# Kernel optimization log

Hardware: AMD Instinct MI355X
Metric: run time of the kernel (lower is better)

Reference implementation:

```python
import jax, jax.numpy as jnp
import numpy as np

CLAMP_MIN = -1.0
CLAMP_MAX = 1.0
EPS = 1e-5


def setup_inputs() -> dict:
    key = jax.random.key(0)
    k1, k2, k3, k4 = jax.random.split(key, 4)
    x = jax.random.normal(k1, (16, 3, 64, 64, 64), dtype=jnp.float32)
    w = jax.random.normal(k2, (16, 3, 3, 3, 3), dtype=jnp.float32) * 0.11  # ~kaiming scale for fan_in=81
    b = jax.random.normal(k3, (16,), dtype=jnp.float32) * 0.1
    m = jax.random.normal(k4, (16, 1, 1, 1), dtype=jnp.float32)
    return {"x": x, "w": w, "b": b, "m": m}


def reference(x, w, b, m):
    # Valid 3D conv: [N,3,D,H,W] x [16,3,3,3,3] -> [N,16,D-2,H-2,W-2]
    y = jax.lax.conv_general_dilated(
        x, w, window_strides=(1, 1, 1), padding='VALID',
        dimension_numbers=('NCDHW', 'OIDHW', 'NCDHW'))
    y = y + b[None, :, None, None, None]
    y = y * m[None]  # per-channel multiply before instance norm
    # InstanceNorm3d (affine=False, biased variance) over spatial dims per (n, c)
    mu = jnp.mean(y, axis=(2, 3, 4), keepdims=True)
    var = jnp.var(y, axis=(2, 3, 4), keepdims=True)
    y = (y - mu) * jax.lax.rsqrt(var + EPS)
    # clamp, second per-channel multiply, then max over channel dim
    y = jnp.clip(y, CLAMP_MIN, CLAMP_MAX) * m[None]
    return jnp.max(y, axis=1)  # [N, D-2, H-2, W-2]
```

## Files before the change

kernel.cpp:

```cpp
#include <hip/hip_runtime.h>
#include <hip/hip_bf16.h>
#include <float.h>

#define DI   64
#define DOUT 62
#define CI   3
#define CO   16
#define NB   16
constexpr int SP    = DOUT * DOUT * DOUT;
constexpr int SP64  = DOUT * DOUT * 64;
constexpr int HT    = 31;
constexpr int DT    = 16;
constexpr int NPART = HT * DT;
constexpr int XDW   = NB * CI * DI * DI * DI / 2;
constexpr int RSTR  = 34;
constexpr int PHD   = 72 * RSTR;

typedef __attribute__((ext_vector_type(8))) short bf16x8;
typedef __attribute__((ext_vector_type(4))) float f32x4;

__device__ float g_psum[NB * CO * NPART];
__device__ float g_psq [NB * CO * NPART];
__device__ float g_stats[NB * CO * 2];
__device__ uint4 g_wb4[4 * 64];
__device__ uint2 g_rt [4 * 64];
__device__ unsigned int g_xbf[XDW];

__device__ __forceinline__ unsigned short f2bf(float v) {
    __hip_bfloat16 h = __float2bfloat16(v);
    return __builtin_bit_cast(unsigned short, h);
}
__device__ __forceinline__ unsigned int pk2(float lo, float hi) {
    return (unsigned int)f2bf(lo) | ((unsigned int)f2bf(hi) << 16);
}

__global__ __launch_bounds__(256) void x2bf_kernel(const float* __restrict__ x,
                                                   const float* __restrict__ w)
{
    if (blockIdx.x == 0) {
        unsigned int* dst = (unsigned int*)g_wb4;
        for (int dwi = threadIdx.x; dwi < 4 * 64 * 4; dwi += 256) {
            const int t    = dwi >> 8;
            const int lane = (dwi >> 2) & 63;
            const int dw   = dwi & 3;
            const int o    = lane & 15, q = lane >> 4;
            const int P    = t * 4 + q;
            unsigned int u = 0;
            for (int half = 0; half < 2; ++half) {
                const int j = dw * 2 + half;
                const int g = (j < 4) ? (2 * P) : (2 * P + 1);
                const int r = j & 3;
                float val = 0.f;
                if (g <= 26 && r < 3) {
                    const int i = g / 9, kd = (g % 9) / 3, kh = g % 3;
                    val = w[o * 81 + i * 27 + kd * 9 + kh * 3 + r];
                }
                u |= ((unsigned int)f2bf(val)) << (16 * half);
            }
            dst[dwi] = u;
        }
        if (threadIdx.x < 256) {
            const int t = threadIdx.x >> 6, lane = threadIdx.x & 63;
            const int q = lane >> 4, P = t * 4 + q;
            uint2 rt;
            const int gA = 2 * P, gB = 2 * P + 1;
            rt.x = (gA <= 26) ? ((gA / 9) * 24 + ((gA % 9) / 3) * 4 + gA % 3) * RSTR : 0;
            rt.y = (gB <= 26) ? ((gB / 9) * 24 + ((gB % 9) / 3) * 4 + gB % 3) * RSTR : 0;
            g_rt[t * 64 + lane] = rt;
        }
    }
    int i = blockIdx.x * 256 + threadIdx.x;
    const int stride = gridDim.x * 256;
    for (; i < XDW / 2; i += stride) {
        const float4 v = ((const float4*)x)[i];
        uint2 u;
        u.x = pk2(v.x, v.y);
        u.y = pk2(v.z, v.w);
        ((uint2*)g_xbf)[i] = u;
    }
}

template <int MODE>
__global__ __launch_bounds__(512) void conv_mfma_kernel(
    const float* __restrict__ m,
    unsigned int* __restrict__ y32, float* __restrict__ out)
{
    __shared__ unsigned int xs[4 * PHD];
    __shared__ float redS[8][CO], redQ[8][CO];

    const int lane = threadIdx.x, ty = threadIdx.y;
    const int h0 = blockIdx.x * 2, d0 = blockIdx.y * 4, n = blockIdx.z;
    const int tid = ty * 64 + lane;

    for (int idx = tid; idx < 72 * 16; idx += 512) {
        const int row = idx >> 4, t = (idx & 15) * 2;
        const int i = row / 24, rm = row % 24, p = rm >> 2, hr = rm & 3;
        const int dg = min(d0 + p, DI - 1);
        const uint2 u = *(const uint2*)(g_xbf +
                          (((n * CI + i) * DI + dg) * DI + (h0 + hr)) * 32 + t);
        const unsigned D2 = __shfl_down(u.x, 1);
        const unsigned D3 = __shfl_down(u.y, 1);
        const unsigned a10 = __builtin_amdgcn_alignbit(u.y, u.x, 16);
        const unsigned a21 = __builtin_amdgcn_alignbit(D2, u.y, 16);
        const unsigned a32 = __builtin_amdgcn_alignbit(D3, D2, 16);
        unsigned int* dp = xs + row * RSTR + t;
        *(uint2*)(dp + 0 * PHD) = u;
        *(uint2*)(dp + 1 * PHD) = make_uint2(a10, a21);
        *(uint2*)(dp + 2 * PHD) = make_uint2(u.y, D2);
        *(uint2*)(dp + 3 * PHD) = make_uint2(a21, a32);
    }
    __syncthreads();

    const int c = lane & 15, q = lane >> 4;
    const int dl = ty >> 1, hl = ty & 1;
    const int offr = ((dl << 2) + hl) * RSTR;

    bf16x8 wf[4];
    int aA[4], aB[4];
#pragma unroll
    for (int t = 0; t < 4; ++t) {
        wf[t] = __builtin_bit_cast(bf16x8, g_wb4[t * 64 + lane]);
        const uint2 rt = g_rt[t * 64 + lane];
        aA[t] = (int)rt.x + offr + 2 * c;
        aB[t] = (int)rt.y + offr + 2 * c;
    }

    const float mc = m[c];
    float A = 0.f, Bp = 0.f;
    if (MODE == 2) {
        A  = g_stats[(n * CO + c) * 2 + 0];
        Bp = g_stats[(n * CO + c) * 2 + 1];
    }

    const int d = d0 + dl, h = h0 + hl;
    const bool dvalid = d < DOUT;
    float sS = 0.f, qS = 0.f;

    if (dvalid) {
        f32x4 acc[4];
#pragma unroll
        for (int wt = 0; wt < 4; ++wt) {
            f32x4 a = {0.f, 0.f, 0.f, 0.f};
#pragma unroll
            for (int t = 0; t < 4; ++t) {
                const uint2 lo = *(const uint2*)(xs + wt * PHD + aA[t]);
                const uint2 hi = *(const uint2*)(xs + wt * PHD + aB[t]);
                uint4 av;
                av.x = lo.x; av.y = lo.y; av.z = hi.x; av.w = hi.y;
                a = __builtin_amdgcn_mfma_f32_16x16x32_bf16(
                        __builtin_bit_cast(bf16x8, av), wf[t], a, 0, 0, 0);
            }
            acc[wt] = a;
        }

        if (MODE == 2) {
            const size_t spb = (size_t)(d * DOUT + h) * DOUT + 16 * q;
#pragma unroll
            for (int reg = 0; reg < 4; ++reg)
#pragma unroll
                for (int wt = 0; wt < 4; ++wt) {
                    const int p = reg * 4 + wt;
                    float z = fminf(fmaxf(fmaf(acc[wt][reg], A, Bp), -1.f), 1.f) * mc;
                    z = fmaxf(z, __shfl_xor(z, 1));
                    z = fmaxf(z, __shfl_xor(z, 2));
                    z = fmaxf(z, __shfl_xor(z, 4));
                    z = fmaxf(z, __shfl_xor(z, 8));
                    if (c == p && (p < 14 || q < 3))
                        out[(size_t)n * SP + spb + p] = z;
                }
        } else {
#pragma unroll
            for (int wt = 0; wt < 4; ++wt)
#pragma unroll
                for (int reg = 0; reg < 4; ++reg) {
                    const float a = acc[wt][reg];
                    sS += a; qS = fmaf(a, a, qS);
                }
            if (q == 3) {
                const float e2 = acc[2][3], e3 = acc[3][3];
                sS -= e2 + e3;
                qS -= fmaf(e2, e2, e3 * e3);
            }
            if (MODE == 1) {
                const size_t ypd = (size_t)(n * CO + c) * (SP64 / 2)
                                 + (size_t)(d * DOUT + h) * 32 + 8 * q;
                uint4 s0, s1;
                s0.x = pk2(acc[0][0], acc[1][0]); s0.y = pk2(acc[2][0], acc[3][0]);
                s0.z = pk2(acc[0][1], acc[1][1]); s0.w = pk2(acc[2][1], acc[3][1]);
                s1.x = pk2(acc[0][2], acc[1][2]); s1.y = pk2(acc[2][2], acc[3][2]);
                s1.z = pk2(acc[0][3], acc[1][3]); s1.w = pk2(acc[2][3], acc[3][3]);
                *(uint4*)(y32 + ypd)     = s0;
                *(uint4*)(y32 + ypd + 4) = s1;
            }
        }
    }

    if (MODE != 2) {
        sS += __shfl_xor(sS, 16); qS += __shfl_xor(qS, 16);
        sS += __shfl_xor(sS, 32); qS += __shfl_xor(qS, 32);
        if (lane < 16) { redS[ty][c] = sS; redQ[ty][c] = qS; }
        __syncthreads();
        if (ty == 0 && lane < 16) {
            float s = 0.f, qq = 0.f;
#pragma unroll
            for (int wv = 0; wv < 8; ++wv) { s += redS[wv][lane]; qq += redQ[wv][lane]; }
            const int blk = blockIdx.y * HT + blockIdx.x;
            g_psum[(n * CO + lane) * NPART + blk] = s;
            g_psq [(n * CO + lane) * NPART + blk] = qq;
        }
    }
}

__global__ __launch_bounds__(256) void finalize_stats_kernel(const float* __restrict__ m)
{
    const int idx = blockIdx.x;
    const int tid = threadIdx.x;
    __shared__ float ls[256], lq[256];
    float s = g_psum[idx * NPART + tid];
    float q = g_psq [idx * NPART + tid];
    if (tid + 256 < NPART) {
        s += g_psum[idx * NPART + tid + 256];
        q += g_psq [idx * NPART + tid + 256];
    }
    ls[tid] = s; lq[tid] = q;
    __syncthreads();
    for (int off = 128; off > 0; off >>= 1) {
        if (tid < off) { ls[tid] += ls[tid + off]; lq[tid] += lq[tid + off]; }
        __syncthreads();
    }
    if (tid == 0) {
        const float inv_n = 1.0f / (float)SP;
        const float muA = ls[0] * inv_n;
        const float varA = fmaxf(lq[0] * inv_n - muA * muA, 0.f);
        const float mo = m[idx & 15];
        const float isv = rsqrtf(fmaf(mo * mo, varA, 1e-5f));
        const float A = mo * isv;
        g_stats[idx * 2 + 0] = A;
        g_stats[idx * 2 + 1] = -muA * A;
    }
}

__global__ __launch_bounds__(256) void pass2_kernel(
    const unsigned int* __restrict__ y32, const float* __restrict__ m,
    float* __restrict__ out)
{
    const int n = blockIdx.y;
    const int t2 = blockIdx.x * 256 + threadIdx.x;
    if (t2 >= DOUT * DOUT * 16) return;
    const int wp2 = t2 & 15;
    const int row = t2 >> 4;
    const float* st = g_stats + n * CO * 2;
    const uint2* yn = (const uint2*)(y32 + (size_t)n * CO * (SP64 / 2)) + t2;
    float mx0 = -FLT_MAX, mx1 = -FLT_MAX, mx2 = -FLT_MAX, mx3 = -FLT_MAX;
#pragma unroll
    for (int o = 0; o < CO; ++o) {
        const uint2 u = yn[(size_t)o * (SP64 / 4)];
        const float A = st[o * 2], Bp = st[o * 2 + 1], mo = m[o];
        float z;
        z = fminf(fmaxf(fmaf(__uint_as_float(u.x << 16),         A, Bp), -1.f), 1.f) * mo;
        mx0 = fmaxf(mx0, z);
        z = fminf(fmaxf(fmaf(__uint_as_float(u.x & 0xFFFF0000u), A, Bp), -1.f), 1.f) * mo;
        mx1 = fmaxf(mx1, z);
        z = fminf(fmaxf(fmaf(__uint_as_float(u.y << 16),         A, Bp), -1.f), 1.f) * mo;
        mx2 = fmaxf(mx2, z);
        z = fminf(fmaxf(fmaf(__uint_as_float(u.y & 0xFFFF0000u), A, Bp), -1.f), 1.f) * mo;
        mx3 = fmaxf(mx3, z);
    }
    float* op = out + (size_t)n * SP + (size_t)row * DOUT + 4 * wp2;
    *(float2*)op = make_float2(mx0, mx1);
    if (wp2 < 15) *(float2*)(op + 2) = make_float2(mx2, mx3);
}

extern "C" void kernel_launch(void* const* d_in, const int* in_sizes, int n_in,
                              void* d_out, int out_size, void* d_ws, size_t ws_size,
                              hipStream_t stream)
{
    const float* x = (const float*)d_in[0];
    const float* w = (const float*)d_in[1];
    const float* m = (const float*)d_in[3];
    float* out = (float*)d_out;

    const dim3 blk(64, 8);
    const dim3 grd(HT, DT, NB);
    const size_t yBytes = (size_t)NB * CO * SP64 * 2;

    x2bf_kernel<<<dim3(2048), dim3(256), 0, stream>>>(x, w);

    if (ws_size >= yBytes) {
        unsigned int* y = (unsigned int*)d_ws;
        conv_mfma_kernel<1><<<grd, blk, 0, stream>>>(m, y, nullptr);
        finalize_stats_kernel<<<dim3(NB * CO), dim3(256), 0, stream>>>(m);
        pass2_kernel<<<dim3((DOUT * DOUT * 16 + 255) / 256, NB), dim3(256), 0, stream>>>(y, m, out);
    } else {
        conv_mfma_kernel<0><<<grd, blk, 0, stream>>>(m, nullptr, nullptr);
        finalize_stats_kernel<<<dim3(NB * CO), dim3(256), 0, stream>>>(m);
        conv_mfma_kernel<2><<<grd, blk, 0, stream>>>(m, nullptr, out);
    }
}
```

Before: 91.12 us.

## Tile four output rows per block and cut shifted LDS copies from four to two

Each block now covers 4 h-rows instead of 2, so the shared input tile holds 6 h-rows per depth slice (108 rows) and the halo is reused across more outputs. Instead of staging four shifted copies of the input in LDS, it stores two (aligned and 1-element shifted) and builds the other two alignments from paired uint2 reads at offsets. The goal is less global-to-LDS staging traffic and fewer LDS writes per output. The cost is extra LDS reads per MFMA and a grid that is half as large, which lowers parallelism. The stats finalize is adjusted to the new 256-partial count.

```diff
diff --git a/kernel.cpp b/kernel.cpp
--- a/kernel.cpp
+++ b/kernel.cpp
@@ -9,12 +9,13 @@
 #define NB   16
 constexpr int SP    = DOUT * DOUT * DOUT;
 constexpr int SP64  = DOUT * DOUT * 64;
-constexpr int HT    = 31;
+constexpr int HT    = 16;
 constexpr int DT    = 16;
 constexpr int NPART = HT * DT;
 constexpr int XDW   = NB * CI * DI * DI * DI / 2;
 constexpr int RSTR  = 34;
-constexpr int PHD   = 72 * RSTR;
+constexpr int ROWS  = 108;
+constexpr int PHD2  = ROWS * RSTR;
 
 typedef __attribute__((ext_vector_type(8))) short bf16x8;
 typedef __attribute__((ext_vector_type(4))) float f32x4;
@@ -64,8 +65,8 @@
             const int q = lane >> 4, P = t * 4 + q;
             uint2 rt;
             const int gA = 2 * P, gB = 2 * P + 1;
-            rt.x = (gA <= 26) ? ((gA / 9) * 24 + ((gA % 9) / 3) * 4 + gA % 3) * RSTR : 0;
-            rt.y = (gB <= 26) ? ((gB / 9) * 24 + ((gB % 9) / 3) * 4 + gB % 3) * RSTR : 0;
+            rt.x = (gA <= 26) ? ((gA / 9) * 36 + ((gA % 9) / 3) * 6 + gA % 3) * RSTR : 0;
+            rt.y = (gB <= 26) ? ((gB / 9) * 36 + ((gB % 9) / 3) * 6 + gB % 3) * RSTR : 0;
             g_rt[t * 64 + lane] = rt;
         }
     }
@@ -85,44 +86,41 @@
     const float* __restrict__ m,
     unsigned int* __restrict__ y32, float* __restrict__ out)
 {
-    __shared__ unsigned int xs[4 * PHD];
+    __shared__ unsigned int xs[2 * PHD2];
     __shared__ float redS[8][CO], redQ[8][CO];
 
     const int lane = threadIdx.x, ty = threadIdx.y;
-    const int h0 = blockIdx.x * 2, d0 = blockIdx.y * 4, n = blockIdx.z;
+    const int h0 = blockIdx.x * 4, d0 = blockIdx.y * 4, n = blockIdx.z;
     const int tid = ty * 64 + lane;
 
-    for (int idx = tid; idx < 72 * 16; idx += 512) {
+    for (int j = tid; j < ROWS * 2; j += 512)
+        *(uint2*)(xs + (j & 1) * PHD2 + (j >> 1) * RSTR + 32) = make_uint2(0u, 0u);
+
+    for (int idx = tid; idx < ROWS * 16; idx += 512) {
         const int row = idx >> 4, t = (idx & 15) * 2;
-        const int i = row / 24, rm = row % 24, p = rm >> 2, hr = rm & 3;
-        const int dg = min(d0 + p, DI - 1);
+        const int i = row / 36, rm = row % 36, pd = rm / 6, hr = rm % 6;
+        const int dg = min(d0 + pd, DI - 1), hg = min(h0 + hr, DI - 1);
         const uint2 u = *(const uint2*)(g_xbf +
-                          (((n * CI + i) * DI + dg) * DI + (h0 + hr)) * 32 + t);
+                          (((n * CI + i) * DI + dg) * DI + hg) * 32 + t);
         const unsigned D2 = __shfl_down(u.x, 1);
-        const unsigned D3 = __shfl_down(u.y, 1);
-        const unsigned a10 = __builtin_amdgcn_alignbit(u.y, u.x, 16);
-        const unsigned a21 = __builtin_amdgcn_alignbit(D2, u.y, 16);
-        const unsigned a32 = __builtin_amdgcn_alignbit(D3, D2, 16);
         unsigned int* dp = xs + row * RSTR + t;
-        *(uint2*)(dp + 0 * PHD) = u;
-        *(uint2*)(dp + 1 * PHD) = make_uint2(a10, a21);
-        *(uint2*)(dp + 2 * PHD) = make_uint2(u.y, D2);
-        *(uint2*)(dp + 3 * PHD) = make_uint2(a21, a32);
+        *(uint2*)dp = u;
+        *(uint2*)(dp + PHD2) = make_uint2(__builtin_amdgcn_alignbit(u.y, u.x, 16),
+                                          __builtin_amdgcn_alignbit(D2, u.y, 16));
     }
     __syncthreads();
 
     const int c = lane & 15, q = lane >> 4;
-    const int dl = ty >> 1, hl = ty & 1;
-    const int offr = ((dl << 2) + hl) * RSTR;
+    const int dl = ty >> 1, hlq = ty & 1;
 
     bf16x8 wf[4];
-    int aA[4], aB[4];
+    int bA[4], bB[4];
 #pragma unroll
     for (int t = 0; t < 4; ++t) {
         wf[t] = __builtin_bit_cast(bf16x8, g_wb4[t * 64 + lane]);
         const uint2 rt = g_rt[t * 64 + lane];
-        aA[t] = (int)rt.x + offr + 2 * c;
-        aB[t] = (int)rt.y + offr + 2 * c;
+        bA[t] = (int)rt.x + 2 * c;
+        bB[t] = (int)rt.y + 2 * c;
     }
 
     const float mc = m[c];
@@ -132,65 +130,84 @@
         Bp = g_stats[(n * CO + c) * 2 + 1];
     }
 
-    const int d = d0 + dl, h = h0 + hl;
+    const int d = d0 + dl;
     const bool dvalid = d < DOUT;
     float sS = 0.f, qS = 0.f;
 
-    if (dvalid) {
-        f32x4 acc[4];
-#pragma unroll
-        for (int wt = 0; wt < 4; ++wt) {
-            f32x4 a = {0.f, 0.f, 0.f, 0.f};
+#pragma unroll
+    for (int r2 = 0; r2 < 2; ++r2) {
+        const int hl = hlq * 2 + r2;
+        const int h = h0 + hl;
+        if (dvalid && h < DOUT) {
+            const int offr = (dl * 6 + hl) * RSTR;
+            f32x4 acc[4];
+#pragma unroll
+            for (int wt = 0; wt < 4; ++wt) acc[wt] = f32x4{0.f, 0.f, 0.f, 0.f};
 #pragma unroll
             for (int t = 0; t < 4; ++t) {
-                const uint2 lo = *(const uint2*)(xs + wt * PHD + aA[t]);
-                const uint2 hi = *(const uint2*)(xs + wt * PHD + aB[t]);
+                const int a = bA[t] + offr, b = bB[t] + offr;
+                const uint2 rA0 = *(const uint2*)(xs + a);
+                const uint2 rA1 = *(const uint2*)(xs + a + 2);
+                const uint2 rB0 = *(const uint2*)(xs + b);
+                const uint2 rB1 = *(const uint2*)(xs + b + 2);
+                const uint2 sA0 = *(const uint2*)(xs + PHD2 + a);
+                const uint2 sA1 = *(const uint2*)(xs + PHD2 + a + 2);
+                const uint2 sB0 = *(const uint2*)(xs + PHD2 + b);
+                const uint2 sB1 = *(const uint2*)(xs + PHD2 + b + 2);
                 uint4 av;
-                av.x = lo.x; av.y = lo.y; av.z = hi.x; av.w = hi.y;
-                a = __builtin_amdgcn_mfma_f32_16x16x32_bf16(
-                        __builtin_bit_cast(bf16x8, av), wf[t], a, 0, 0, 0);
+                av = make_uint4(rA0.x, rA0.y, rB0.x, rB0.y);
+                acc[0] = __builtin_amdgcn_mfma_f32_16x16x32_bf16(
+                             __builtin_bit_cast(bf16x8, av), wf[t], acc[0], 0, 0, 0);
+                av = make_uint4(sA0.x, sA0.y, sB0.x, sB0.y);
+                acc[1] = __builtin_amdgcn_mfma_f32_16x16x32_bf16(
+                             __builtin_bit_cast(bf16x8, av), wf[t], acc[1], 0, 0, 0);
+                av = make_uint4(rA0.y, rA1.x, rB0.y, rB1.x);
+                acc[2] = __builtin_amdgcn_mfma_f32_16x16x32_bf16(
+                             __builtin_bit_cast(bf16x8, av), wf[t], acc[2], 0, 0, 0);
+                av = make_uint4(sA0.y, sA1.x, sB0.y, sB1.x);
+                acc[3] = __builtin_amdgcn_mfma_f32_16x16x32_bf16(
+                             __builtin_bit_cast(bf16x8, av), wf[t], acc[3], 0, 0, 0);
             }
-            acc[wt] = a;
-        }
-
-        if (MODE == 2) {
-            const size_t spb = (size_t)(d * DOUT + h) * DOUT + 16 * q;
-#pragma unroll
-            for (int reg = 0; reg < 4; ++reg)
-#pragma unroll
-                for (int wt = 0; wt < 4; ++wt) {
-                    const int p = reg * 4 + wt;
-                    float z = fminf(fmaxf(fmaf(acc[wt][reg], A, Bp), -1.f), 1.f) * mc;
-                    z = fmaxf(z, __shfl_xor(z, 1));
-                    z = fmaxf(z, __shfl_xor(z, 2));
-                    z = fmaxf(z, __shfl_xor(z, 4));
-                    z = fmaxf(z, __shfl_xor(z, 8));
-                    if (c == p && (p < 14 || q < 3))
-                        out[(size_t)n * SP + spb + p] = z;
+
+            if (MODE == 2) {
+                const size_t spb = (size_t)(d * DOUT + h) * DOUT + 16 * q;
+#pragma unroll
+                for (int reg = 0; reg < 4; ++reg)
+#pragma unroll
+                    for (int wt = 0; wt < 4; ++wt) {
+                        const int p = reg * 4 + wt;
+                        float z = fminf(fmaxf(fmaf(acc[wt][reg], A, Bp), -1.f), 1.f) * mc;
+                        z = fmaxf(z, __shfl_xor(z, 1));
+                        z = fmaxf(z, __shfl_xor(z, 2));
+                        z = fmaxf(z, __shfl_xor(z, 4));
+                        z = fmaxf(z, __shfl_xor(z, 8));
+                        if (c == p && (p < 14 || q < 3))
+                            out[(size_t)n * SP + spb + p] = z;
+                    }
+            } else {
+#pragma unroll
+                for (int wt = 0; wt < 4; ++wt)
+#pragma unroll
+                    for (int reg = 0; reg < 4; ++reg) {
+                        const float a2 = acc[wt][reg];
+                        sS += a2; qS = fmaf(a2, a2, qS);
+                    }
+                if (q == 3) {
+                    const float e2 = acc[2][3], e3 = acc[3][3];
+                    sS -= e2 + e3;
+                    qS -= fmaf(e2, e2, e3 * e3);
                 }
-        } else {
-#pragma unroll
-            for (int wt = 0; wt < 4; ++wt)
-#pragma unroll
-                for (int reg = 0; reg < 4; ++reg) {
-                    const float a = acc[wt][reg];
-                    sS += a; qS = fmaf(a, a, qS);
+                if (MODE == 1) {
+                    const size_t ypd = (size_t)(n * CO + c) * (SP64 / 2)
+                                     + (size_t)(d * DOUT + h) * 32 + 8 * q;
+                    uint4 s0, s1;
+                    s0.x = pk2(acc[0][0], acc[1][0]); s0.y = pk2(acc[2][0], acc[3][0]);
+                    s0.z = pk2(acc[0][1], acc[1][1]); s0.w = pk2(acc[2][1], acc[3][1]);
+                    s1.x = pk2(acc[0][2], acc[1][2]); s1.y = pk2(acc[2][2], acc[3][2]);
+                    s1.z = pk2(acc[0][3], acc[1][3]); s1.w = pk2(acc[2][3], acc[3][3]);
+                    *(uint4*)(y32 + ypd)     = s0;
+                    *(uint4*)(y32 + ypd + 4) = s1;
                 }
-            if (q == 3) {
-                const float e2 = acc[2][3], e3 = acc[3][3];
-                sS -= e2 + e3;
-                qS -= fmaf(e2, e2, e3 * e3);
-            }
-            if (MODE == 1) {
-                const size_t ypd = (size_t)(n * CO + c) * (SP64 / 2)
-                                 + (size_t)(d * DOUT + h) * 32 + 8 * q;
-                uint4 s0, s1;
-                s0.x = pk2(acc[0][0], acc[1][0]); s0.y = pk2(acc[2][0], acc[3][0]);
-                s0.z = pk2(acc[0][1], acc[1][1]); s0.w = pk2(acc[2][1], acc[3][1]);
-                s1.x = pk2(acc[0][2], acc[1][2]); s1.y = pk2(acc[2][2], acc[3][2]);
-                s1.z = pk2(acc[0][3], acc[1][3]); s1.w = pk2(acc[2][3], acc[3][3]);
-                *(uint4*)(y32 + ypd)     = s0;
-                *(uint4*)(y32 + ypd + 4) = s1;
             }
         }
     }
@@ -216,13 +233,8 @@
     const int idx = blockIdx.x;
     const int tid = threadIdx.x;
     __shared__ float ls[256], lq[256];
-    float s = g_psum[idx * NPART + tid];
-    float q = g_psq [idx * NPART + tid];
-    if (tid + 256 < NPART) {
-        s += g_psum[idx * NPART + tid + 256];
-        q += g_psq [idx * NPART + tid + 256];
-    }
-    ls[tid] = s; lq[tid] = q;
+    ls[tid] = g_psum[idx * NPART + tid];
+    lq[tid] = g_psq [idx * NPART + tid];
     __syncthreads();
     for (int off = 128; off > 0; off >>= 1) {
         if (tid < off) { ls[tid] += ls[tid + off]; lq[tid] += lq[tid + off]; }
```

Result: faster. 82.61 us (-9.3%).
